# Kernel optimization log

Measured on AMD Instinct MI355X. Metric: run time of the kernel, lower is better.

## Reference

```python
import jax, jax.numpy as jnp
import numpy as np

N_NODES = 100000
N_EDGES = 600000
N_REL = 4
N_HEADS = 4
DIM = 128  # in_dim == out_dim (required by out = zeros_like(x) + index_add_ of out_dim msgs)
HEAD_DIM = DIM // N_HEADS
NEG_SLOPE = 0.2


def setup_inputs() -> dict:
    key = jax.random.key(0)
    k1, k2, k3, k4, k5 = jax.random.split(key, 5)
    x = jax.random.normal(k1, (N_NODES, DIM), dtype=jnp.float32)
    edge_index = jax.random.randint(k2, (2, N_EDGES), 0, N_NODES, dtype=jnp.int64)
    edge_types = jax.random.randint(k3, (N_EDGES,), 0, N_REL, dtype=jnp.int64)
    # per-relation linear weights, xavier-ish scale
    W = jax.random.normal(k4, (N_REL, DIM, DIM), dtype=jnp.float32) * (1.0 / np.sqrt(DIM))
    # attention vectors [R, H, 2*head_dim]
    attn = jax.random.normal(k5, (N_REL, N_HEADS, 2 * HEAD_DIM), dtype=jnp.float32) * 0.1
    return {"x": x, "edge_index": edge_index, "edge_types": edge_types, "W": W, "attn": attn}


def reference(x, edge_index, edge_types, W, attn):
    N = x.shape[0]
    R, H, twoD = attn.shape
    D = twoD // 2
    E = edge_types.shape[0]

    # per-relation linear transform: [R, N, H, D]
    x_rel = jnp.einsum('ni,rio->rno', x, W).reshape(R, N, H, D)

    src, dst = edge_index[0], edge_index[1]

    # gather per-edge features with the edge's relation
    src_feat = x_rel[edge_types, src]            # [E, H, D]
    dst_feat = x_rel[edge_types, dst]            # [E, H, D]
    a = attn[edge_types]                         # [E, H, 2D]

    # attention logits + LeakyReLU(0.2)
    cat = jnp.concatenate([src_feat, dst_feat], axis=-1)  # [E, H, 2D]
    alpha = jnp.sum(cat * a, axis=-1)                     # [E, H]
    alpha = jnp.where(alpha > 0, alpha, NEG_SLOPE * alpha)

    # segment softmax over edges sharing (relation, dst)
    seg = edge_types * N + dst                            # [E]
    S = R * N
    m = jax.ops.segment_max(alpha, seg, num_segments=S)   # [S, H]
    alpha_exp = jnp.exp(alpha - m[seg])
    denom = jax.ops.segment_sum(alpha_exp, seg, num_segments=S)
    w = alpha_exp / denom[seg]                            # [E, H]

    # weighted messages, scatter-add to dst
    msg = (src_feat * w[..., None]).reshape(E, H * D)     # [E, out_dim]
    out = jax.ops.segment_sum(msg, dst, num_segments=N)   # [N, out_dim]
    return out
```

## Files before the change

kernel.cpp:

```cpp
#include <hip/hip_runtime.h>
#include <hip/hip_bf16.h>
#include <stdint.h>

#define N_NODES 100000
#define N_EDGES 600000
#define N_REL 4
#define N_HEADS 4
#define DIM 128
#define HEAD_DIM 32
#define NEG_SLOPE 0.2f

typedef unsigned int uint;
typedef unsigned short ushort;
typedef __attribute__((ext_vector_type(8))) short bf16x8;
typedef __attribute__((ext_vector_type(4))) float f32x4;

__device__ __forceinline__ float bf2f(ushort u) { return __uint_as_float(((uint)u) << 16); }
__device__ __forceinline__ float lo2f(uint u) { return __uint_as_float(u << 16); }
__device__ __forceinline__ float hi2f(uint u) { return __uint_as_float(u & 0xffff0000u); }
__device__ __forceinline__ ushort f2bf(float f) {
    uint u = __float_as_uint(f);
    uint r = (u + 0x7fffu + ((u >> 16) & 1u)) >> 16;
    return (ushort)r;
}
__device__ __forceinline__ float lrelu(float v) { return v > 0.f ? v : NEG_SLOPE * v; }

__device__ __forceinline__ int bf16_plaus(ushort u) {
    int ex = (u >> 7) & 0xFF;
    return (ex >= 100 && ex <= 140) ? 1 : 0;
}
__global__ void k_detect(const ushort* __restrict__ x, const ushort* __restrict__ W,
                         const ushort* __restrict__ attn, const int* __restrict__ ei,
                         const int* __restrict__ et, int* __restrict__ flags) {
    __shared__ int cnt[5];
    int t = threadIdx.x;
    if (t < 5) cnt[t] = 0;
    __syncthreads();
    if (t < 128) {
        atomicAdd(&cnt[0], bf16_plaus(x[2 * t]));
        atomicAdd(&cnt[1], bf16_plaus(W[2 * t]));
        atomicAdd(&cnt[2], bf16_plaus(attn[2 * t]));
        atomicAdd(&cnt[3], (ei[2 * t + 1] != 0) ? 1 : 0);
        atomicAdd(&cnt[4], (et[2 * t + 1] != 0) ? 1 : 0);
    }
    __syncthreads();
    if (t == 0) {
        flags[0] = (cnt[0] < 64) ? 1 : 0;
        flags[1] = (cnt[1] < 64) ? 1 : 0;
        flags[2] = (cnt[2] < 64) ? 1 : 0;
        flags[3] = (cnt[3] < 8) ? 1 : 0;
        flags[4] = (cnt[4] < 8) ? 1 : 0;
    }
}

__global__ __launch_bounds__(256) void k_canon_i(
    const int* __restrict__ src, int* __restrict__ dst, int n,
    const int* __restrict__ flags, int flagIdx) {
    int i0 = (blockIdx.x * 256 + threadIdx.x) * 4;
    int i64f = flags[flagIdx];
#pragma unroll
    for (int j = 0; j < 4; j++) {
        int i = i0 + j;
        if (i < n) dst[i] = i64f ? src[2 * i] : src[i];
    }
}

__global__ __launch_bounds__(256) void k_cvt_x(
    const void* __restrict__ xv, const int* __restrict__ flags,
    ushort* __restrict__ x_bf)
{
    int t = blockIdx.x * 256 + threadIdx.x;
    if (t >= N_NODES * DIM / 8) return;
    if (flags[0]) {
        const float4* p = (const float4*)xv + (size_t)t * 2;
        float4 f0 = p[0], f1 = p[1];
        uint4 o;
        o.x = (uint)f2bf(f0.x) | ((uint)f2bf(f0.y) << 16);
        o.y = (uint)f2bf(f0.z) | ((uint)f2bf(f0.w) << 16);
        o.z = (uint)f2bf(f1.x) | ((uint)f2bf(f1.y) << 16);
        o.w = (uint)f2bf(f1.z) | ((uint)f2bf(f1.w) << 16);
        ((uint4*)x_bf)[t] = o;
    } else {
        ((uint4*)x_bf)[t] = ((const uint4*)xv)[t];
    }
}

__global__ __launch_bounds__(256) void k_prep_w(
    const void* __restrict__ Wv, const void* __restrict__ av,
    const int* __restrict__ flags,
    ushort* __restrict__ Wt_g, ushort* __restrict__ at_g)
{
    __shared__ ushort wt[128][136];
    const int r = blockIdx.x;
    const int tid = threadIdx.x;
    const int wf = flags[1], af = flags[2];

    if (wf) {
        const float4* Wg = (const float4*)((const float*)Wv + (size_t)r * DIM * DIM);
        for (int it = 0; it < 16; ++it) {
            int idx = tid + it * 256;
            int k = idx >> 5, n4 = (idx & 31) * 4;
            float4 v = Wg[idx];
            wt[n4 + 0][k] = f2bf(v.x);
            wt[n4 + 1][k] = f2bf(v.y);
            wt[n4 + 2][k] = f2bf(v.z);
            wt[n4 + 3][k] = f2bf(v.w);
        }
    } else {
        const ushort* Wg = (const ushort*)Wv + (size_t)r * DIM * DIM;
        for (int it = 0; it < 16; ++it) {
            int idx = tid + it * 256;
            int k = idx >> 5, n4 = (idx & 31) * 4;
            const ushort* p = Wg + (size_t)k * DIM + n4;
            wt[n4 + 0][k] = p[0];
            wt[n4 + 1][k] = p[1];
            wt[n4 + 2][k] = p[2];
            wt[n4 + 3][k] = p[3];
        }
    }
    __syncthreads();

    for (int it = 0; it < 9; ++it) {
        int idx = tid + it * 256;
        if (idx < 2176) {
            int row = idx / 17, c8 = (idx % 17) * 8;
            *(uint4*)(Wt_g + ((size_t)r * 128 + row) * 136 + c8) = *(const uint4*)&wt[row][c8];
        }
    }
    for (int it = 0; it < 9; ++it) {
        int idx = tid + it * 256;
        if (idx < 16 * 136) {
            int n = idx / 136, k = idx % 136;
            int h = n & 3, sd = (n >> 2) & 1;
            float v = 0.f;
            if (n < 8 && k < 128) {
                int d = k - h * 32;
                if (d >= 0 && d < 32) {
                    size_t ai = ((size_t)(r * N_HEADS + h)) * 64 + (size_t)sd * 32 + d;
                    v = af ? ((const float*)av)[ai] : bf2f(((const ushort*)av)[ai]);
                }
            }
            at_g[((size_t)r * 16 + n) * 136 + k] = f2bf(v);
        }
    }
}

__global__ __launch_bounds__(256) void k_gemm_mfma(
    const ushort* __restrict__ x_bf, const ushort* __restrict__ Wt_g,
    const ushort* __restrict__ at_g,
    ushort* __restrict__ x_rel, float* __restrict__ sTab)
{
    __shared__ ushort wt[128][136];
    __shared__ ushort at[16][136];

    const int tid = threadIdx.x;
    const int wave = tid >> 6, lane = tid & 63;
    const int quad = lane >> 4, l16 = lane & 15;
    const int r = blockIdx.x & 3;
    const int n0 = (blockIdx.x >> 2) * 128;

    {
        const uint4* src  = (const uint4*)(Wt_g + (size_t)r * 128 * 136);
        const uint4* srcA = (const uint4*)(at_g + (size_t)r * 16 * 136);
        uint4* dstL = (uint4*)&wt[0][0];
        uint4* dstA = (uint4*)&at[0][0];
#pragma unroll
        for (int it = 0; it < 10; ++it) {
            int idx = tid + it * 256;
            if (idx < 2176) dstL[idx] = src[idx];
            else if (idx < 2448) dstA[idx - 2176] = srcA[idx - 2176];
        }
    }

    const int rowA0 = n0 + wave * 32 + l16;
    const int rowA1 = rowA0 + 16;
    const size_t rA0 = (size_t)min(rowA0, N_NODES - 1) * DIM;
    const size_t rA1 = (size_t)min(rowA1, N_NODES - 1) * DIM;

    __syncthreads();

    f32x4 acc[2][8];
#pragma unroll
    for (int rt = 0; rt < 2; ++rt)
#pragma unroll
        for (int ct = 0; ct < 8; ++ct) acc[rt][ct] = (f32x4){0.f, 0.f, 0.f, 0.f};

#pragma unroll
    for (int q = 0; q < 4; ++q) {
        const int kb = q * 32 + quad * 8;
        bf16x8 a0 = *(const bf16x8*)(x_bf + rA0 + kb);
        bf16x8 a1 = *(const bf16x8*)(x_bf + rA1 + kb);
#pragma unroll
        for (int ct = 0; ct < 8; ++ct) {
            bf16x8 b = *(const bf16x8*)&wt[ct * 16 + l16][kb];
            acc[0][ct] = __builtin_amdgcn_mfma_f32_16x16x32_bf16(a0, b, acc[0][ct], 0, 0, 0);
            acc[1][ct] = __builtin_amdgcn_mfma_f32_16x16x32_bf16(a1, b, acc[1][ct], 0, 0, 0);
        }
    }
    __syncthreads();

    {
        ushort* rp = &wt[0][0];
#pragma unroll
        for (int rt = 0; rt < 2; ++rt) {
            int rowb = wave * 32 + rt * 16 + quad * 4;
#pragma unroll
            for (int ct = 0; ct < 8; ++ct) {
                int col = ct * 16 + l16;
#pragma unroll
                for (int reg = 0; reg < 4; ++reg)
                    rp[(rowb + reg) * 136 + col] = f2bf(acc[rt][ct][reg]);
            }
        }
    }
    __syncthreads();

    {
        const ushort* rp = &wt[0][0];
        f32x4 sacc[2];
        sacc[0] = (f32x4){0.f, 0.f, 0.f, 0.f};
        sacc[1] = (f32x4){0.f, 0.f, 0.f, 0.f};
#pragma unroll
        for (int q = 0; q < 4; ++q) {
            const int kb = q * 32 + quad * 8;
            bf16x8 a0 = *(const bf16x8*)(rp + (wave * 32 + l16) * 136 + kb);
            bf16x8 a1 = *(const bf16x8*)(rp + (wave * 32 + 16 + l16) * 136 + kb);
            bf16x8 bat = *(const bf16x8*)&at[l16][kb];
            sacc[0] = __builtin_amdgcn_mfma_f32_16x16x32_bf16(a0, bat, sacc[0], 0, 0, 0);
            sacc[1] = __builtin_amdgcn_mfma_f32_16x16x32_bf16(a1, bat, sacc[1], 0, 0, 0);
        }
        if (l16 < 8) {
#pragma unroll
            for (int rt = 0; rt < 2; ++rt) {
#pragma unroll
                for (int reg = 0; reg < 4; ++reg) {
                    int node = n0 + wave * 32 + rt * 16 + quad * 4 + reg;
                    if (node < N_NODES)
                        sTab[((size_t)r * N_NODES + node) * 8 + l16] = sacc[rt][reg];
                }
            }
        }
    }

    {
        const ushort* rp = &wt[0][0];
        const size_t rbase = (size_t)r * N_NODES * DIM;
#pragma unroll
        for (int p = 0; p < 8; ++p) {
            int row = p * 16 + (tid >> 4);
            int chunk = tid & 15;
            int node = n0 + row;
            if (node < N_NODES) {
                uint4 v = *(const uint4*)(rp + row * 136 + chunk * 8);
                *(uint4*)(x_rel + rbase + (size_t)node * DIM + chunk * 8) = v;
            }
        }
    }
}

__global__ __launch_bounds__(256) void k_hist(
    const int* __restrict__ ei, uint* __restrict__ deg)
{
    int e = blockIdx.x * 256 + threadIdx.x;
    if (e >= N_EDGES) return;
    atomicAdd(&deg[ei[N_EDGES + e]], 1u);
}

__global__ __launch_bounds__(256) void k_scan1(
    const uint* __restrict__ deg, uint* __restrict__ excl, uint* __restrict__ bsum)
{
    __shared__ uint tmp[256];
    int i = blockIdx.x * 256 + threadIdx.x;
    uint v = (i < N_NODES) ? deg[i] : 0u;
    tmp[threadIdx.x] = v;
    __syncthreads();
    for (int off = 1; off < 256; off <<= 1) {
        uint t = (threadIdx.x >= off) ? tmp[threadIdx.x - off] : 0u;
        __syncthreads();
        tmp[threadIdx.x] += t;
        __syncthreads();
    }
    if (i < N_NODES) excl[i] = tmp[threadIdx.x] - v;
    if (threadIdx.x == 255) bsum[blockIdx.x] = tmp[255];
}

__global__ __launch_bounds__(512) void k_scan2(uint* __restrict__ bsum, int nblocks)
{
    __shared__ uint tmp[512];
    int t = threadIdx.x;
    uint v = (t < nblocks) ? bsum[t] : 0u;
    tmp[t] = v;
    __syncthreads();
    for (int off = 1; off < 512; off <<= 1) {
        uint tt = (t >= off) ? tmp[t - off] : 0u;
        __syncthreads();
        tmp[t] += tt;
        __syncthreads();
    }
    if (t < nblocks) bsum[t] = tmp[t] - v;
}

__global__ __launch_bounds__(256) void k_scan3(
    const uint* __restrict__ excl, const uint* __restrict__ bsum,
    uint* __restrict__ start, uint* __restrict__ cursor)
{
    int i = blockIdx.x * 256 + threadIdx.x;
    if (i >= N_NODES) return;
    uint s = excl[i] + bsum[blockIdx.x];
    start[i] = s;
    cursor[i] = s;
}

__global__ __launch_bounds__(256) void k_fill(
    const int* __restrict__ ei, const int* __restrict__ et,
    uint* __restrict__ cursor, uint* __restrict__ csrPack)
{
    int e = blockIdx.x * 256 + threadIdx.x;
    if (e >= N_EDGES) return;
    int s = ei[e];
    int d = ei[N_EDGES + e];
    int r = et[e];
    uint pos = atomicAdd(&cursor[d], 1u);
    csrPack[pos] = (uint)s | ((uint)r << 27);
}


#define EDGE_LOAD(J) \
    uint sx##J = pk##J & 0x07FFFFFFu; \
    uint re##J = pk##J >> 27; \
    size_t rb##J = (size_t)re##J * N_NODES + sx##J; \
    float4 aV##J = *(const float4*)(sTab + rb##J * 8); \
    uint u##J = x_rel_u[rb##J * 64 + lane];

#define EDGE_ACC(J, VLD) { \
    float ah = (h < 2) ? (h == 0 ? aV##J.x : aV##J.y) : (h == 2 ? aV##J.z : aV##J.w); \
    float bb = (re##J < 2) ? (re##J == 0 ? b0 : b1) : (re##J == 2 ? b2 : b3); \
    float y = __expf(lrelu(ah + bb)); \
    y = (VLD) ? y : 0.f; \
    float xlo = lo2f(u##J), xhi = hi2f(u##J); \
    float m0 = (re##J == 0) ? y : 0.f; \
    float m1 = (re##J == 1) ? y : 0.f; \
    float m2 = (re##J == 2) ? y : 0.f; \
    float m3 = (re##J == 3) ? y : 0.f; \
    ds0 += m0; ds1 += m1; ds2 += m2; ds3 += m3; \
    a0l = fmaf(m0, xlo, a0l); a0h = fmaf(m0, xhi, a0h); \
    a1l = fmaf(m1, xlo, a1l); a1h = fmaf(m1, xhi, a1h); \
    a2l = fmaf(m2, xlo, a2l); a2h = fmaf(m2, xhi, a2h); \
    a3l = fmaf(m3, xlo, a3l); a3h = fmaf(m3, xhi, a3h); \
}

__global__ __launch_bounds__(256) void k_gather3(
    const uint* __restrict__ start, const uint* __restrict__ deg,
    const uint* __restrict__ csrPack, const float* __restrict__ sTab,
    const uint* __restrict__ x_rel_u, float* __restrict__ out)
{
    const int wv = threadIdx.x >> 6;
    const int dst = blockIdx.x * 4 + wv;
    if (dst >= N_NODES) return;
    const int lane = threadIdx.x & 63;
    const int h = lane >> 4;

    const uint st = start[dst];
    const uint dg = deg[dst];

    float4 q0 = *(const float4*)(sTab + ((size_t)0 * N_NODES + dst) * 8 + 4);
    float4 q1 = *(const float4*)(sTab + ((size_t)1 * N_NODES + dst) * 8 + 4);
    float4 q2 = *(const float4*)(sTab + ((size_t)2 * N_NODES + dst) * 8 + 4);
    float4 q3 = *(const float4*)(sTab + ((size_t)3 * N_NODES + dst) * 8 + 4);
    float b0 = (h < 2) ? (h == 0 ? q0.x : q0.y) : (h == 2 ? q0.z : q0.w);
    float b1 = (h < 2) ? (h == 0 ? q1.x : q1.y) : (h == 2 ? q1.z : q1.w);
    float b2 = (h < 2) ? (h == 0 ? q2.x : q2.y) : (h == 2 ? q2.z : q2.w);
    float b3 = (h < 2) ? (h == 0 ? q3.x : q3.y) : (h == 2 ? q3.z : q3.w);

    float a0l = 0.f, a0h = 0.f, a1l = 0.f, a1h = 0.f;
    float a2l = 0.f, a2h = 0.f, a3l = 0.f, a3h = 0.f;
    float ds0 = 0.f, ds1 = 0.f, ds2 = 0.f, ds3 = 0.f;

    if (dg != 0u) {
        const uint last = st + dg - 1u;
        for (uint e0 = 0; e0 < dg; e0 += 4) {
            uint i0 = st + e0;
            uint i1 = (i0 + 1u <= last) ? i0 + 1u : last;
            uint i2 = (i0 + 2u <= last) ? i0 + 2u : last;
            uint i3 = (i0 + 3u <= last) ? i0 + 3u : last;
            uint pk0 = csrPack[i0];
            uint pk1 = csrPack[i1];
            uint pk2 = csrPack[i2];
            uint pk3 = csrPack[i3];
            EDGE_LOAD(0) EDGE_LOAD(1) EDGE_LOAD(2) EDGE_LOAD(3)
            EDGE_ACC(0, 1)
            EDGE_ACC(1, e0 + 1u < dg)
            EDGE_ACC(2, e0 + 2u < dg)
            EDGE_ACC(3, e0 + 3u < dg)
        }
    }

    float rs0 = (ds0 > 0.f) ? 1.f / ds0 : 0.f;
    float rs1 = (ds1 > 0.f) ? 1.f / ds1 : 0.f;
    float rs2 = (ds2 > 0.f) ? 1.f / ds2 : 0.f;
    float rs3 = (ds3 > 0.f) ? 1.f / ds3 : 0.f;

    float2 o;
    o.x = a0l * rs0 + a1l * rs1 + a2l * rs2 + a3l * rs3;
    o.y = a0h * rs0 + a1h * rs1 + a2h * rs2 + a3h * rs3;
    *(float2*)(out + (size_t)dst * DIM + lane * 2) = o;
}

extern "C" void kernel_launch(void* const* d_in, const int* in_sizes, int n_in,
                              void* d_out, int out_size, void* d_ws, size_t ws_size,
                              hipStream_t stream) {
    const void* x    = d_in[0];
    const int*  ei   = (const int*)d_in[1];
    const int*  et   = (const int*)d_in[2];
    const void* W    = d_in[3];
    const void* attn = d_in[4];
    float* out = (float*)d_out;

    char* ws = (char*)d_ws;
    int*    flags   = (int*)(ws + 0);
    int*    eic     = (int*)(ws + 256);
    int*    etc_    = (int*)(ws + 4800256);
    float*  sTab    = (float*)(ws + 7200256);
    ushort* x_rel   = (ushort*)(ws + 20000256);
    uint*   deg     = (uint*)(ws + 122400256);
    uint*   excl    = (uint*)(ws + 122800256);
    uint*   bsum    = (uint*)(ws + 123200256);
    uint*   startA  = (uint*)(ws + 123202304);
    uint*   cursor  = (uint*)(ws + 123602304);
    uint*   csrPack = (uint*)(ws + 124002304);
    ushort* x_bf    = (ushort*)(ws + 126402304);
    ushort* Wt_g    = (ushort*)(ws + 122800256);
    ushort* at_g    = (ushort*)(ws + 123202304);

    const int NBLK = (N_NODES + 255) / 256;

    hipMemsetAsync(deg, 0, 400000, stream);

    k_detect<<<1, 256, 0, stream>>>((const ushort*)x, (const ushort*)W,
                                    (const ushort*)attn, ei, et, flags);
    k_prep_w<<<N_REL, 256, 0, stream>>>(W, attn, flags, Wt_g, at_g);
    k_canon_i<<<(2 * N_EDGES / 4 + 255) / 256, 256, 0, stream>>>(ei, eic, 2 * N_EDGES, flags, 3);
    k_canon_i<<<(N_EDGES / 4 + 255) / 256, 256, 0, stream>>>(et, etc_, N_EDGES, flags, 4);
    k_cvt_x<<<(N_NODES * DIM / 8 + 255) / 256, 256, 0, stream>>>(x, flags, x_bf);

    k_gemm_mfma<<<((N_NODES + 127) / 128) * N_REL, 256, 0, stream>>>(x_bf, Wt_g, at_g,
                                                                     x_rel, sTab);

    k_hist<<<(N_EDGES + 255) / 256, 256, 0, stream>>>(eic, deg);
    k_scan1<<<NBLK, 256, 0, stream>>>(deg, excl, bsum);
    k_scan2<<<1, 512, 0, stream>>>(bsum, NBLK);
    k_scan3<<<NBLK, 256, 0, stream>>>(excl, bsum, startA, cursor);
    k_fill<<<(N_EDGES + 255) / 256, 256, 0, stream>>>(eic, etc_, cursor, csrPack);
    k_gather3<<<(N_NODES + 3) / 4, 256, 0, stream>>>(startA, deg, csrPack, sTab,
                                                     (const uint*)x_rel, out);
}
```

Baseline: 327.6 us.

## Precompute per-edge attention exps and softmax denominators in edge pass

Moves the exp/leaky-relu attention logit computation out of the per-destination gather into the edge histogram kernel. That kernel now writes per-edge exp values and atomically accumulates per-(relation,dst,head) denominators. The gather then needs only one accumulator pair per lane instead of four relation-split pairs. In exchange it adds float atomics, a 6.4MB memset, a wider CSR entry (edge id) and an extra random yTab load per edge in the gather.

```diff
diff --git a/kernel.cpp b/kernel.cpp
--- a/kernel.cpp
+++ b/kernel.cpp
@@ -258,12 +258,30 @@
     }
 }
 
-__global__ __launch_bounds__(256) void k_hist(
-    const int* __restrict__ ei, uint* __restrict__ deg)
+__global__ __launch_bounds__(256) void k_denom(
+    const int* __restrict__ eic, const int* __restrict__ etc_,
+    const float* __restrict__ sTab,
+    float* __restrict__ dTab, float* __restrict__ yTab, uint* __restrict__ deg)
 {
     int e = blockIdx.x * 256 + threadIdx.x;
     if (e >= N_EDGES) return;
-    atomicAdd(&deg[ei[N_EDGES + e]], 1u);
+    int s = eic[e];
+    int d = eic[N_EDGES + e];
+    int r = etc_[e];
+    atomicAdd(&deg[d], 1u);
+    float4 a = *(const float4*)(sTab + ((size_t)r * N_NODES + s) * 8);
+    float4 b = *(const float4*)(sTab + ((size_t)r * N_NODES + d) * 8 + 4);
+    float4 y;
+    y.x = __expf(lrelu(a.x + b.x));
+    y.y = __expf(lrelu(a.y + b.y));
+    y.z = __expf(lrelu(a.z + b.z));
+    y.w = __expf(lrelu(a.w + b.w));
+    *(float4*)(yTab + (size_t)e * 4) = y;
+    float* dp = dTab + ((size_t)r * N_NODES + d) * 4;
+    atomicAdd(dp + 0, y.x);
+    atomicAdd(dp + 1, y.y);
+    atomicAdd(dp + 2, y.z);
+    atomicAdd(dp + 3, y.w);
 }
 
 __global__ __launch_bounds__(256) void k_scan1(
@@ -312,46 +330,23 @@
 }
 
 __global__ __launch_bounds__(256) void k_fill(
-    const int* __restrict__ ei, const int* __restrict__ et,
-    uint* __restrict__ cursor, uint* __restrict__ csrPack)
+    const int* __restrict__ eic, const int* __restrict__ etc_,
+    uint* __restrict__ cursor, uint2* __restrict__ csrPack2)
 {
     int e = blockIdx.x * 256 + threadIdx.x;
     if (e >= N_EDGES) return;
-    int s = ei[e];
-    int d = ei[N_EDGES + e];
-    int r = et[e];
+    int s = eic[e];
+    int d = eic[N_EDGES + e];
+    int r = etc_[e];
     uint pos = atomicAdd(&cursor[d], 1u);
-    csrPack[pos] = (uint)s | ((uint)r << 27);
-}
-
-
-#define EDGE_LOAD(J) \
-    uint sx##J = pk##J & 0x07FFFFFFu; \
-    uint re##J = pk##J >> 27; \
-    size_t rb##J = (size_t)re##J * N_NODES + sx##J; \
-    float4 aV##J = *(const float4*)(sTab + rb##J * 8); \
-    uint u##J = x_rel_u[rb##J * 64 + lane];
-
-#define EDGE_ACC(J, VLD) { \
-    float ah = (h < 2) ? (h == 0 ? aV##J.x : aV##J.y) : (h == 2 ? aV##J.z : aV##J.w); \
-    float bb = (re##J < 2) ? (re##J == 0 ? b0 : b1) : (re##J == 2 ? b2 : b3); \
-    float y = __expf(lrelu(ah + bb)); \
-    y = (VLD) ? y : 0.f; \
-    float xlo = lo2f(u##J), xhi = hi2f(u##J); \
-    float m0 = (re##J == 0) ? y : 0.f; \
-    float m1 = (re##J == 1) ? y : 0.f; \
-    float m2 = (re##J == 2) ? y : 0.f; \
-    float m3 = (re##J == 3) ? y : 0.f; \
-    ds0 += m0; ds1 += m1; ds2 += m2; ds3 += m3; \
-    a0l = fmaf(m0, xlo, a0l); a0h = fmaf(m0, xhi, a0h); \
-    a1l = fmaf(m1, xlo, a1l); a1h = fmaf(m1, xhi, a1h); \
-    a2l = fmaf(m2, xlo, a2l); a2h = fmaf(m2, xhi, a2h); \
-    a3l = fmaf(m3, xlo, a3l); a3h = fmaf(m3, xhi, a3h); \
-}
-
-__global__ __launch_bounds__(256) void k_gather3(
+    uint2 pk; pk.x = (uint)s | ((uint)r << 27); pk.y = (uint)e;
+    csrPack2[pos] = pk;
+}
+
+__global__ __launch_bounds__(256) void k_gather4(
     const uint* __restrict__ start, const uint* __restrict__ deg,
-    const uint* __restrict__ csrPack, const float* __restrict__ sTab,
+    const uint2* __restrict__ csrPack2, const float* __restrict__ dTab,
+    const float* __restrict__ yTab,
     const uint* __restrict__ x_rel_u, float* __restrict__ out)
 {
     const int wv = threadIdx.x >> 6;
@@ -363,18 +358,16 @@
     const uint st = start[dst];
     const uint dg = deg[dst];
 
-    float4 q0 = *(const float4*)(sTab + ((size_t)0 * N_NODES + dst) * 8 + 4);
-    float4 q1 = *(const float4*)(sTab + ((size_t)1 * N_NODES + dst) * 8 + 4);
-    float4 q2 = *(const float4*)(sTab + ((size_t)2 * N_NODES + dst) * 8 + 4);
-    float4 q3 = *(const float4*)(sTab + ((size_t)3 * N_NODES + dst) * 8 + 4);
-    float b0 = (h < 2) ? (h == 0 ? q0.x : q0.y) : (h == 2 ? q0.z : q0.w);
-    float b1 = (h < 2) ? (h == 0 ? q1.x : q1.y) : (h == 2 ? q1.z : q1.w);
-    float b2 = (h < 2) ? (h == 0 ? q2.x : q2.y) : (h == 2 ? q2.z : q2.w);
-    float b3 = (h < 2) ? (h == 0 ? q3.x : q3.y) : (h == 2 ? q3.z : q3.w);
-
-    float a0l = 0.f, a0h = 0.f, a1l = 0.f, a1h = 0.f;
-    float a2l = 0.f, a2h = 0.f, a3l = 0.f, a3h = 0.f;
-    float ds0 = 0.f, ds1 = 0.f, ds2 = 0.f, ds3 = 0.f;
+    float d0 = dTab[((size_t)0 * N_NODES + dst) * 4 + h];
+    float d1 = dTab[((size_t)1 * N_NODES + dst) * 4 + h];
+    float d2 = dTab[((size_t)2 * N_NODES + dst) * 4 + h];
+    float d3 = dTab[((size_t)3 * N_NODES + dst) * 4 + h];
+    float rs0 = (d0 > 0.f) ? 1.f / d0 : 0.f;
+    float rs1 = (d1 > 0.f) ? 1.f / d1 : 0.f;
+    float rs2 = (d2 > 0.f) ? 1.f / d2 : 0.f;
+    float rs3 = (d3 > 0.f) ? 1.f / d3 : 0.f;
+
+    float a0 = 0.f, a1 = 0.f;
 
     if (dg != 0u) {
         const uint last = st + dg - 1u;
@@ -383,26 +376,38 @@
             uint i1 = (i0 + 1u <= last) ? i0 + 1u : last;
             uint i2 = (i0 + 2u <= last) ? i0 + 2u : last;
             uint i3 = (i0 + 3u <= last) ? i0 + 3u : last;
-            uint pk0 = csrPack[i0];
-            uint pk1 = csrPack[i1];
-            uint pk2 = csrPack[i2];
-            uint pk3 = csrPack[i3];
-            EDGE_LOAD(0) EDGE_LOAD(1) EDGE_LOAD(2) EDGE_LOAD(3)
-            EDGE_ACC(0, 1)
-            EDGE_ACC(1, e0 + 1u < dg)
-            EDGE_ACC(2, e0 + 2u < dg)
-            EDGE_ACC(3, e0 + 3u < dg)
-        }
-    }
-
-    float rs0 = (ds0 > 0.f) ? 1.f / ds0 : 0.f;
-    float rs1 = (ds1 > 0.f) ? 1.f / ds1 : 0.f;
-    float rs2 = (ds2 > 0.f) ? 1.f / ds2 : 0.f;
-    float rs3 = (ds3 > 0.f) ? 1.f / ds3 : 0.f;
-
-    float2 o;
-    o.x = a0l * rs0 + a1l * rs1 + a2l * rs2 + a3l * rs3;
-    o.y = a0h * rs0 + a1h * rs1 + a2h * rs2 + a3h * rs3;
+            uint2 pk0 = csrPack2[i0];
+            uint2 pk1 = csrPack2[i1];
+            uint2 pk2 = csrPack2[i2];
+            uint2 pk3 = csrPack2[i3];
+            float y0 = yTab[(size_t)pk0.y * 4 + h];
+            float y1 = yTab[(size_t)pk1.y * 4 + h];
+            float y2 = yTab[(size_t)pk2.y * 4 + h];
+            float y3 = yTab[(size_t)pk3.y * 4 + h];
+            uint re0 = pk0.x >> 27, sx0 = pk0.x & 0x07FFFFFFu;
+            uint re1 = pk1.x >> 27, sx1 = pk1.x & 0x07FFFFFFu;
+            uint re2 = pk2.x >> 27, sx2 = pk2.x & 0x07FFFFFFu;
+            uint re3 = pk3.x >> 27, sx3 = pk3.x & 0x07FFFFFFu;
+            uint u0 = x_rel_u[((size_t)re0 * N_NODES + sx0) * 64 + lane];
+            uint u1 = x_rel_u[((size_t)re1 * N_NODES + sx1) * 64 + lane];
+            uint u2 = x_rel_u[((size_t)re2 * N_NODES + sx2) * 64 + lane];
+            uint u3 = x_rel_u[((size_t)re3 * N_NODES + sx3) * 64 + lane];
+            float rsA = (re0 < 2) ? (re0 == 0 ? rs0 : rs1) : (re0 == 2 ? rs2 : rs3);
+            float rsB = (re1 < 2) ? (re1 == 0 ? rs0 : rs1) : (re1 == 2 ? rs2 : rs3);
+            float rsC = (re2 < 2) ? (re2 == 0 ? rs0 : rs1) : (re2 == 2 ? rs2 : rs3);
+            float rsD = (re3 < 2) ? (re3 == 0 ? rs0 : rs1) : (re3 == 2 ? rs2 : rs3);
+            float mw0 = y0 * rsA;
+            float mw1 = (e0 + 1u < dg) ? y1 * rsB : 0.f;
+            float mw2 = (e0 + 2u < dg) ? y2 * rsC : 0.f;
+            float mw3 = (e0 + 3u < dg) ? y3 * rsD : 0.f;
+            a0 = fmaf(mw0, lo2f(u0), a0); a1 = fmaf(mw0, hi2f(u0), a1);
+            a0 = fmaf(mw1, lo2f(u1), a0); a1 = fmaf(mw1, hi2f(u1), a1);
+            a0 = fmaf(mw2, lo2f(u2), a0); a1 = fmaf(mw2, hi2f(u2), a1);
+            a0 = fmaf(mw3, lo2f(u3), a0); a1 = fmaf(mw3, hi2f(u3), a1);
+        }
+    }
+
+    float2 o; o.x = a0; o.y = a1;
     *(float2*)(out + (size_t)dst * DIM + lane * 2) = o;
 }
 
@@ -427,10 +432,12 @@
     uint*   bsum    = (uint*)(ws + 123200256);
     uint*   startA  = (uint*)(ws + 123202304);
     uint*   cursor  = (uint*)(ws + 123602304);
-    uint*   csrPack = (uint*)(ws + 124002304);
     ushort* x_bf    = (ushort*)(ws + 126402304);
     ushort* Wt_g    = (ushort*)(ws + 122800256);
     ushort* at_g    = (ushort*)(ws + 123202304);
+    float*  dTab    = (float*)(ws + 126402304);
+    float*  yTab    = (float*)(ws + 132802304);
+    uint2*  csrPack2= (uint2*)(ws + 142402304);
 
     const int NBLK = (N_NODES + 255) / 256;
 
@@ -446,11 +453,12 @@
     k_gemm_mfma<<<((N_NODES + 127) / 128) * N_REL, 256, 0, stream>>>(x_bf, Wt_g, at_g,
                                                                      x_rel, sTab);
 
-    k_hist<<<(N_EDGES + 255) / 256, 256, 0, stream>>>(eic, deg);
+    hipMemsetAsync(dTab, 0, 6400000, stream);
+    k_denom<<<(N_EDGES + 255) / 256, 256, 0, stream>>>(eic, etc_, sTab, dTab, yTab, deg);
     k_scan1<<<NBLK, 256, 0, stream>>>(deg, excl, bsum);
     k_scan2<<<1, 512, 0, stream>>>(bsum, NBLK);
     k_scan3<<<NBLK, 256, 0, stream>>>(excl, bsum, startA, cursor);
-    k_fill<<<(N_EDGES + 255) / 256, 256, 0, stream>>>(eic, etc_, cursor, csrPack);
-    k_gather3<<<(N_NODES + 3) / 4, 256, 0, stream>>>(startA, deg, csrPack, sTab,
+    k_fill<<<(N_EDGES + 255) / 256, 256, 0, stream>>>(eic, etc_, cursor, csrPack2);
+    k_gather4<<<(N_NODES + 3) / 4, 256, 0, stream>>>(startA, deg, csrPack2, dTab, yTab,
                                                      (const uint*)x_rel, out);
 }
```

Result: slower. 426.1 us (+30.0%).
